# Optimization experiments

Measured on AMD Instinct MI355X. Metric: run time of the kernel, lower is better.

## Reference

```python
import jax, jax.numpy as jnp
import numpy as np

B, N, D = 8, 4096, 3

def setup_inputs() -> dict:
    key = jax.random.key(0)
    kx, ky = jax.random.split(key)
    x = jax.random.normal(kx, (B, N, D), dtype=jnp.float32)
    y = jax.random.normal(ky, (B, N, D), dtype=jnp.float32)
    return {"x": x, "y": y}

def _nn_diff(A, B_):
    # brute-force NN: squared distances [N, M] via ||a||^2 + ||b||^2 - 2 a.b
    a2 = jnp.sum(A * A, axis=-1)[:, None]
    b2 = jnp.sum(B_ * B_, axis=-1)[None, :]
    d2 = a2 + b2 - 2.0 * (A @ B_.T)
    idx = jnp.argmin(d2, axis=1)            # closest point in B_ for each point in A
    return A - B_[idx]                      # [N, D] signed residuals

def _sigma_pair(S1, S2):
    d12 = _nn_diff(S1, S2)                  # S1 -> S2 residuals
    d21 = _nn_diff(S2, S1)                  # S2 -> S1 residuals
    # torch.std over the whole [N, D] tensor with Bessel's correction (ddof=1)
    std1 = jnp.std(d12, ddof=1)
    std2 = jnp.std(d21, ddof=1)
    return jnp.maximum(std1, std2)

def reference(x, y):
    per_batch = jax.vmap(_sigma_pair)(x, y)  # [B]
    return per_batch.mean()
```

## Files before the change

kernel.cpp:

```cpp
#include <hip/hip_runtime.h>
#include <math.h>

#define NPTS 4096
#define BLK 256
#define NUNITS 16
#define QGRP 128
#define QGRPS 32
#define GRID1 (NUNITS * QGRPS)
#define PHT 2048
#define CNT 12288.0f

typedef _Float16 half8 __attribute__((ext_vector_type(8)));
typedef float f32x16 __attribute__((ext_vector_type(16)));

__device__ __forceinline__ unsigned umin2(unsigned a, unsigned b) { return a < b ? a : b; }
__device__ __forceinline__ float fmin3(float a, float b, float c) {
  return fminf(fminf(a, b), c);
}

__device__ __forceinline__ float tilemin16(const f32x16 d) {
  const float a0 = fmin3(d[0],  d[1],  d[2]);
  const float a1 = fmin3(d[3],  d[4],  d[5]);
  const float a2 = fmin3(d[6],  d[7],  d[8]);
  const float a3 = fmin3(d[9],  d[10], d[11]);
  const float a4 = fmin3(d[12], d[13], d[14]);
  return fminf(fmin3(a0, a1, a2), fmin3(a3, a4, d[15]));
}

__global__ __launch_bounds__(BLK, 2) void fullscan_kernel(
    const float* __restrict__ x, const float* __restrict__ y,
    float2* __restrict__ partials) {
  __shared__ half8 Ap[2 * PHT];
  __shared__ half8 Bq[2 * QGRP];
  __shared__ float wS[4], wSS[4];

  const int bid  = blockIdx.x;
  const int unit = bid >> 5, qg = bid & 31;
  const int b = unit >> 1, dir = unit & 1;
  const float* __restrict__ Q = (dir ? y : x) + (size_t)b * NPTS * 3;
  const float* __restrict__ T = (dir ? x : y) + (size_t)b * NPTS * 3;

  const int tid = threadIdx.x;
  const _Float16 one  = (_Float16)1.0f;
  const _Float16 zero = (_Float16)0.0f;
  const _Float16 n2   = (_Float16)(-2.0f);

  if (tid < QGRP) {
    const int qq = qg * QGRP + tid;
    const float ax = Q[3 * qq], ay = Q[3 * qq + 1], az = Q[3 * qq + 2];
    const float a2 = fmaf(ax, ax, fmaf(ay, ay, az * az));
    const _Float16 ah0 = (_Float16)ax, ah1 = (_Float16)ay, ah2 = (_Float16)az;
    const _Float16 al0 = (_Float16)(ax - (float)ah0);
    const _Float16 al1 = (_Float16)(ay - (float)ah1);
    const _Float16 al2 = (_Float16)(az - (float)ah2);
    const _Float16 a2h = (_Float16)a2;
    const _Float16 a2l = (_Float16)(a2 - (float)a2h);
    half8 lo, hi;
    lo[0] = n2 * ah0; lo[1] = n2 * ah1; lo[2] = n2 * ah2; lo[3] = n2 * ah0;
    lo[4] = n2 * ah1; lo[5] = n2 * ah2; lo[6] = n2 * al0; lo[7] = n2 * al1;
    hi[0] = n2 * al2; hi[1] = one; hi[2] = one; hi[3] = a2h;
    hi[4] = a2l; hi[5] = zero; hi[6] = zero; hi[7] = zero;
    Bq[tid]        = lo;
    Bq[QGRP + tid] = hi;
  }

  const int lane = tid & 63, w = tid >> 6, ln = lane & 31, hi5 = lane >> 5;
  unsigned kacc0 = 0xFFFFFFFFu, kacc1 = 0xFFFFFFFFu;
  f32x16 Z;
  #pragma unroll
  for (int r = 0; r < 16; ++r) Z[r] = 0.0f;

  half8 bf;
  for (int c = 0; c < 2; ++c) {
    __syncthreads();
    #pragma unroll
    for (int k = 0; k < 8; ++k) {
      const int i  = tid + k * BLK;
      const int tg = c * PHT + i;
      const float bx = T[3 * tg], by = T[3 * tg + 1], bz = T[3 * tg + 2];
      const float b2 = fmaf(bx, bx, fmaf(by, by, bz * bz));
      const _Float16 bh0 = (_Float16)bx, bh1 = (_Float16)by, bh2 = (_Float16)bz;
      const _Float16 bl0 = (_Float16)(bx - (float)bh0);
      const _Float16 bl1 = (_Float16)(by - (float)bh1);
      const _Float16 bl2 = (_Float16)(bz - (float)bh2);
      const _Float16 s2h = (_Float16)b2;
      const _Float16 s2l = (_Float16)(b2 - (float)s2h);
      half8 lo, hi;
      lo[0] = bh0; lo[1] = bh1; lo[2] = bh2; lo[3] = bl0;
      lo[4] = bl1; lo[5] = bl2; lo[6] = bh0; lo[7] = bh1;
      hi[0] = bh2; hi[1] = s2h; hi[2] = s2l; hi[3] = one;
      hi[4] = one; hi[5] = zero; hi[6] = zero; hi[7] = zero;
      Ap[i]       = lo;
      Ap[PHT + i] = hi;
    }
    __syncthreads();
    if (c == 0) bf = Bq[hi5 * QGRP + w * 32 + ln];

    const unsigned cb = (unsigned)(c * (PHT / 32));
    #pragma unroll 4
    for (int t = 0; t < PHT / 32; ++t) {
      const half8 af = Ap[hi5 * PHT + t * 32 + ln];
      const f32x16 d = __builtin_amdgcn_mfma_f32_32x32x16_f16(af, bf, Z, 0, 0, 0);
      const unsigned key = (__float_as_uint(tilemin16(d)) & 0xFFFFF000u) | (cb + (unsigned)t);
      if (t & 1) kacc1 = umin2(kacc1, key);
      else       kacc0 = umin2(kacc0, key);
    }
  }
  unsigned kacc = umin2(kacc0, kacc1);
  kacc = umin2(kacc, (unsigned)__shfl_xor((int)kacc, 32));

  float s = 0.f, ss = 0.f;
  if (lane < 32) {
    const int q = qg * QGRP + w * 32 + ln;
    const int tbase = (int)(kacc & 4095u) * 32;
    const float qx = Q[3 * q], qy = Q[3 * q + 1], qz = Q[3 * q + 2];
    unsigned best = 0xFFFFFFFFu;
    #pragma unroll 8
    for (int i = 0; i < 32; ++i) {
      const int j = tbase + i;
      const float dx = qx - T[3 * j];
      const float dy = qy - T[3 * j + 1];
      const float dz = qz - T[3 * j + 2];
      const float d2 = fmaf(dx, dx, fmaf(dy, dy, dz * dz));
      best = umin2(best, (__float_as_uint(d2) & 0xFFFFFFE0u) | (unsigned)i);
    }
    const int j = tbase + (int)(best & 31u);
    const float rx = qx - T[3 * j];
    const float ry = qy - T[3 * j + 1];
    const float rz = qz - T[3 * j + 2];
    s  = rx + ry + rz;
    ss = fmaf(rx, rx, fmaf(ry, ry, rz * rz));
  }

  #pragma unroll
  for (int off = 32; off > 0; off >>= 1) {
    s  += __shfl_down(s, off);
    ss += __shfl_down(ss, off);
  }
  if ((tid & 63) == 0) { wS[w] = s; wSS[w] = ss; }
  __syncthreads();
  if (tid == 0) {
    partials[bid] = make_float2(wS[0] + wS[1] + wS[2] + wS[3],
                                wSS[0] + wSS[1] + wSS[2] + wSS[3]);
  }
}

__global__ __launch_bounds__(BLK) void finalize_kernel(
    const float2* __restrict__ partials, float* __restrict__ out) {
  __shared__ float2 sh[GRID1];
  __shared__ float sig[NUNITS];

  sh[threadIdx.x]       = partials[threadIdx.x];
  sh[threadIdx.x + BLK] = partials[threadIdx.x + BLK];
  __syncthreads();

  if (threadIdx.x < NUNITS) {
    float S = 0.f, SS = 0.f;
    #pragma unroll
    for (int i = 0; i < QGRPS; ++i) {
      S  += sh[threadIdx.x * QGRPS + i].x;
      SS += sh[threadIdx.x * QGRPS + i].y;
    }
    const float var = (SS - S * S / CNT) / (CNT - 1.0f);
    sig[threadIdx.x] = sqrtf(fmaxf(var, 0.0f));
  }
  __syncthreads();

  if (threadIdx.x == 0) {
    float acc = 0.f;
    #pragma unroll
    for (int b = 0; b < 8; ++b) acc += fmaxf(sig[2 * b], sig[2 * b + 1]);
    out[0] = acc * 0.125f;
  }
}

extern "C" void kernel_launch(void* const* d_in, const int* in_sizes, int n_in,
                              void* d_out, int out_size, void* d_ws, size_t ws_size,
                              hipStream_t stream) {
  const float* x = (const float*)d_in[0];
  const float* y = (const float*)d_in[1];
  float* out = (float*)d_out;
  float2* partials = (float2*)d_ws;

  hipLaunchKernelGGL(fullscan_kernel, dim3(GRID1), dim3(BLK), 0, stream,
                     x, y, partials);
  hipLaunchKernelGGL(finalize_kernel, dim3(1), dim3(BLK), 0, stream,
                     partials, out);
}
```

Before: 23.30 us.

## Precompute fp16 MFMA operands in a pack kernel and prefetch target phases into registers

Adds a pack kernel that converts every point set once into its hi/lo fp16 MFMA operand layout. Before, each of the 512 blocks redid this conversion for all 4096 target points. The scan kernel now loads the packed operands and splits the targets into four phases of 1024. The next phase is prefetched into registers while the current phase's MFMAs run, which halves LDS use. In exchange it adds a kernel launch, about 2 MB of workspace traffic, and extra barriers per phase.

```diff
diff --git a/kernel.cpp b/kernel.cpp
--- a/kernel.cpp
+++ b/kernel.cpp
@@ -7,8 +7,11 @@
 #define QGRP 128
 #define QGRPS 32
 #define GRID1 (NUNITS * QGRPS)
-#define PHT 2048
+#define PHT 1024
+#define NPH 4
 #define CNT 12288.0f
+#define PACK_HALF8 (8 * 2 * 2 * 4096)
+#define PACK_BYTES ((size_t)PACK_HALF8 * 16)
 
 typedef _Float16 half8 __attribute__((ext_vector_type(8)));
 typedef float f32x16 __attribute__((ext_vector_type(16)));
@@ -27,8 +30,47 @@
   return fminf(fmin3(a0, a1, a2), fmin3(a3, a4, d[15]));
 }
 
+__global__ __launch_bounds__(BLK) void pack_kernel(
+    const float* __restrict__ x, const float* __restrict__ y,
+    half8* __restrict__ Apk, half8* __restrict__ Bpk) {
+  const int gid = blockIdx.x * BLK + threadIdx.x;
+  const int b   = gid >> 13;
+  const int set = (gid >> 12) & 1;
+  const int i   = gid & 4095;
+  const float* __restrict__ P = (set ? y : x) + (size_t)b * NPTS * 3;
+
+  const float px = P[3 * i], py = P[3 * i + 1], pz = P[3 * i + 2];
+  const float p2 = fmaf(px, px, fmaf(py, py, pz * pz));
+  const _Float16 h0 = (_Float16)px, h1 = (_Float16)py, h2 = (_Float16)pz;
+  const _Float16 l0 = (_Float16)(px - (float)h0);
+  const _Float16 l1 = (_Float16)(py - (float)h1);
+  const _Float16 l2 = (_Float16)(pz - (float)h2);
+  const _Float16 s2h = (_Float16)p2;
+  const _Float16 s2l = (_Float16)(p2 - (float)s2h);
+  const _Float16 one  = (_Float16)1.0f;
+  const _Float16 zero = (_Float16)0.0f;
+  const _Float16 n2   = (_Float16)(-2.0f);
+
+  half8 alo, ahi, blo, bhi;
+  alo[0] = h0; alo[1] = h1; alo[2] = h2; alo[3] = l0;
+  alo[4] = l1; alo[5] = l2; alo[6] = h0; alo[7] = h1;
+  ahi[0] = h2; ahi[1] = s2h; ahi[2] = s2l; ahi[3] = one;
+  ahi[4] = one; ahi[5] = zero; ahi[6] = zero; ahi[7] = zero;
+  blo[0] = n2 * h0; blo[1] = n2 * h1; blo[2] = n2 * h2; blo[3] = n2 * h0;
+  blo[4] = n2 * h1; blo[5] = n2 * h2; blo[6] = n2 * l0; blo[7] = n2 * l1;
+  bhi[0] = n2 * l2; bhi[1] = one; bhi[2] = one; bhi[3] = s2h;
+  bhi[4] = s2l; bhi[5] = zero; bhi[6] = zero; bhi[7] = zero;
+
+  const size_t base = (size_t)((b * 2 + set) * 2) * 4096 + i;
+  Apk[base]        = alo;
+  Apk[base + 4096] = ahi;
+  Bpk[base]        = blo;
+  Bpk[base + 4096] = bhi;
+}
+
 __global__ __launch_bounds__(BLK, 2) void fullscan_kernel(
     const float* __restrict__ x, const float* __restrict__ y,
+    const half8* __restrict__ Apk, const half8* __restrict__ Bpk,
     float2* __restrict__ partials) {
   __shared__ half8 Ap[2 * PHT];
   __shared__ half8 Bq[2 * QGRP];
@@ -39,71 +81,61 @@
   const int b = unit >> 1, dir = unit & 1;
   const float* __restrict__ Q = (dir ? y : x) + (size_t)b * NPTS * 3;
   const float* __restrict__ T = (dir ? x : y) + (size_t)b * NPTS * 3;
+  const half8* __restrict__ Ab = Apk + (size_t)((b * 2 + (1 - dir)) * 2) * 4096;
+  const half8* __restrict__ Bb = Bpk + (size_t)((b * 2 + dir) * 2) * 4096;
 
   const int tid = threadIdx.x;
-  const _Float16 one  = (_Float16)1.0f;
-  const _Float16 zero = (_Float16)0.0f;
-  const _Float16 n2   = (_Float16)(-2.0f);
-
-  if (tid < QGRP) {
-    const int qq = qg * QGRP + tid;
-    const float ax = Q[3 * qq], ay = Q[3 * qq + 1], az = Q[3 * qq + 2];
-    const float a2 = fmaf(ax, ax, fmaf(ay, ay, az * az));
-    const _Float16 ah0 = (_Float16)ax, ah1 = (_Float16)ay, ah2 = (_Float16)az;
-    const _Float16 al0 = (_Float16)(ax - (float)ah0);
-    const _Float16 al1 = (_Float16)(ay - (float)ah1);
-    const _Float16 al2 = (_Float16)(az - (float)ah2);
-    const _Float16 a2h = (_Float16)a2;
-    const _Float16 a2l = (_Float16)(a2 - (float)a2h);
-    half8 lo, hi;
-    lo[0] = n2 * ah0; lo[1] = n2 * ah1; lo[2] = n2 * ah2; lo[3] = n2 * ah0;
-    lo[4] = n2 * ah1; lo[5] = n2 * ah2; lo[6] = n2 * al0; lo[7] = n2 * al1;
-    hi[0] = n2 * al2; hi[1] = one; hi[2] = one; hi[3] = a2h;
-    hi[4] = a2l; hi[5] = zero; hi[6] = zero; hi[7] = zero;
-    Bq[tid]        = lo;
-    Bq[QGRP + tid] = hi;
-  }
+
+  {
+    const int plane = tid >> 7, qi = tid & 127;
+    Bq[plane * QGRP + qi] = Bb[(size_t)plane * 4096 + qg * QGRP + qi];
+  }
+  #pragma unroll
+  for (int k = 0; k < 8; ++k) {
+    const int e = k * BLK + tid;
+    const int plane = e >> 10, ti = e & 1023;
+    Ap[plane * PHT + ti] = Ab[(size_t)plane * 4096 + ti];
+  }
+  __syncthreads();
 
   const int lane = tid & 63, w = tid >> 6, ln = lane & 31, hi5 = lane >> 5;
-  unsigned kacc0 = 0xFFFFFFFFu, kacc1 = 0xFFFFFFFFu;
+  const half8 bf = Bq[hi5 * QGRP + w * 32 + ln];
+
   f32x16 Z;
   #pragma unroll
   for (int r = 0; r < 16; ++r) Z[r] = 0.0f;
 
-  half8 bf;
-  for (int c = 0; c < 2; ++c) {
-    __syncthreads();
-    #pragma unroll
-    for (int k = 0; k < 8; ++k) {
-      const int i  = tid + k * BLK;
-      const int tg = c * PHT + i;
-      const float bx = T[3 * tg], by = T[3 * tg + 1], bz = T[3 * tg + 2];
-      const float b2 = fmaf(bx, bx, fmaf(by, by, bz * bz));
-      const _Float16 bh0 = (_Float16)bx, bh1 = (_Float16)by, bh2 = (_Float16)bz;
-      const _Float16 bl0 = (_Float16)(bx - (float)bh0);
-      const _Float16 bl1 = (_Float16)(by - (float)bh1);
-      const _Float16 bl2 = (_Float16)(bz - (float)bh2);
-      const _Float16 s2h = (_Float16)b2;
-      const _Float16 s2l = (_Float16)(b2 - (float)s2h);
-      half8 lo, hi;
-      lo[0] = bh0; lo[1] = bh1; lo[2] = bh2; lo[3] = bl0;
-      lo[4] = bl1; lo[5] = bl2; lo[6] = bh0; lo[7] = bh1;
-      hi[0] = bh2; hi[1] = s2h; hi[2] = s2l; hi[3] = one;
-      hi[4] = one; hi[5] = zero; hi[6] = zero; hi[7] = zero;
-      Ap[i]       = lo;
-      Ap[PHT + i] = hi;
-    }
-    __syncthreads();
-    if (c == 0) bf = Bq[hi5 * QGRP + w * 32 + ln];
-
+  unsigned kacc0 = 0xFFFFFFFFu, kacc1 = 0xFFFFFFFFu;
+  half8 nxt[8];
+
+  for (int c = 0; c < NPH; ++c) {
+    if (c < NPH - 1) {
+      #pragma unroll
+      for (int k = 0; k < 8; ++k) {
+        const int e = k * BLK + tid;
+        const int plane = e >> 10, ti = e & 1023;
+        nxt[k] = Ab[(size_t)plane * 4096 + (c + 1) * PHT + ti];
+      }
+    }
     const unsigned cb = (unsigned)(c * (PHT / 32));
     #pragma unroll 4
     for (int t = 0; t < PHT / 32; ++t) {
       const half8 af = Ap[hi5 * PHT + t * 32 + ln];
       const f32x16 d = __builtin_amdgcn_mfma_f32_32x32x16_f16(af, bf, Z, 0, 0, 0);
-      const unsigned key = (__float_as_uint(tilemin16(d)) & 0xFFFFF000u) | (cb + (unsigned)t);
+      const unsigned key =
+          (__float_as_uint(tilemin16(d)) & 0xFFFFF000u) | (cb + (unsigned)t);
       if (t & 1) kacc1 = umin2(kacc1, key);
       else       kacc0 = umin2(kacc0, key);
+    }
+    __syncthreads();
+    if (c < NPH - 1) {
+      #pragma unroll
+      for (int k = 0; k < 8; ++k) {
+        const int e = k * BLK + tid;
+        const int plane = e >> 10, ti = e & 1023;
+        Ap[plane * PHT + ti] = nxt[k];
+      }
+      __syncthreads();
     }
   }
   unsigned kacc = umin2(kacc0, kacc1);
@@ -180,10 +212,16 @@
   const float* x = (const float*)d_in[0];
   const float* y = (const float*)d_in[1];
   float* out = (float*)d_out;
-  float2* partials = (float2*)d_ws;
-
+
+  char* ws = (char*)d_ws;
+  half8* Apk = (half8*)ws;
+  half8* Bpk = (half8*)(ws + PACK_BYTES);
+  float2* partials = (float2*)(ws + 2 * PACK_BYTES);
+
+  hipLaunchKernelGGL(pack_kernel, dim3(65536 / BLK), dim3(BLK), 0, stream,
+                     x, y, Apk, Bpk);
   hipLaunchKernelGGL(fullscan_kernel, dim3(GRID1), dim3(BLK), 0, stream,
-                     x, y, partials);
+                     x, y, Apk, Bpk, partials);
   hipLaunchKernelGGL(finalize_kernel, dim3(1), dim3(BLK), 0, stream,
                      partials, out);
 }
```

New measurement: 29.48 us. 26.6% more time.

## Split target scan across two waves per query tile with 512-thread blocks

Applied to the files above, without the earlier changes.

Doubles the block to 512 threads so that two waves share each 32-query tile, each scanning half of the target points in every chunk. Their packed min keys are merged through shared memory before a single wave refines the result. This halves the serial MFMA loop per wave and raises the number of waves in flight, which is meant to hide latency. The cost is an extra barrier plus shared-memory exchange, and higher register pressure because launch bounds now ask for 4 blocks of 512 threads.

```diff
diff --git a/kernel.cpp b/kernel.cpp
--- a/kernel.cpp
+++ b/kernel.cpp
@@ -2,7 +2,7 @@
 #include <math.h>
 
 #define NPTS 4096
-#define BLK 256
+#define BLK2 512
 #define NUNITS 16
 #define QGRP 128
 #define QGRPS 32
@@ -27,12 +27,13 @@
   return fminf(fmin3(a0, a1, a2), fmin3(a3, a4, d[15]));
 }
 
-__global__ __launch_bounds__(BLK, 2) void fullscan_kernel(
+__global__ __launch_bounds__(BLK2, 4) void fullscan_kernel(
     const float* __restrict__ x, const float* __restrict__ y,
     float2* __restrict__ partials) {
   __shared__ half8 Ap[2 * PHT];
   __shared__ half8 Bq[2 * QGRP];
-  __shared__ float wS[4], wSS[4];
+  __shared__ unsigned km[4][32];
+  __shared__ float wS[8], wSS[8];
 
   const int bid  = blockIdx.x;
   const int unit = bid >> 5, qg = bid & 31;
@@ -45,8 +46,9 @@
   const _Float16 zero = (_Float16)0.0f;
   const _Float16 n2   = (_Float16)(-2.0f);
 
-  if (tid < QGRP) {
-    const int qq = qg * QGRP + tid;
+  if (tid < 2 * QGRP) {
+    const int plane = tid >> 7, qi = tid & 127;
+    const int qq = qg * QGRP + qi;
     const float ax = Q[3 * qq], ay = Q[3 * qq + 1], az = Q[3 * qq + 2];
     const float a2 = fmaf(ax, ax, fmaf(ay, ay, az * az));
     const _Float16 ah0 = (_Float16)ax, ah1 = (_Float16)ay, ah2 = (_Float16)az;
@@ -55,16 +57,19 @@
     const _Float16 al2 = (_Float16)(az - (float)ah2);
     const _Float16 a2h = (_Float16)a2;
     const _Float16 a2l = (_Float16)(a2 - (float)a2h);
-    half8 lo, hi;
-    lo[0] = n2 * ah0; lo[1] = n2 * ah1; lo[2] = n2 * ah2; lo[3] = n2 * ah0;
-    lo[4] = n2 * ah1; lo[5] = n2 * ah2; lo[6] = n2 * al0; lo[7] = n2 * al1;
-    hi[0] = n2 * al2; hi[1] = one; hi[2] = one; hi[3] = a2h;
-    hi[4] = a2l; hi[5] = zero; hi[6] = zero; hi[7] = zero;
-    Bq[tid]        = lo;
-    Bq[QGRP + tid] = hi;
+    half8 v;
+    if (plane == 0) {
+      v[0] = n2 * ah0; v[1] = n2 * ah1; v[2] = n2 * ah2; v[3] = n2 * ah0;
+      v[4] = n2 * ah1; v[5] = n2 * ah2; v[6] = n2 * al0; v[7] = n2 * al1;
+    } else {
+      v[0] = n2 * al2; v[1] = one; v[2] = one; v[3] = a2h;
+      v[4] = a2l; v[5] = zero; v[6] = zero; v[7] = zero;
+    }
+    Bq[plane * QGRP + qi] = v;
   }
 
   const int lane = tid & 63, w = tid >> 6, ln = lane & 31, hi5 = lane >> 5;
+  const int qt = w >> 1, th = w & 1;
   unsigned kacc0 = 0xFFFFFFFFu, kacc1 = 0xFFFFFFFFu;
   f32x16 Z;
   #pragma unroll
@@ -74,8 +79,8 @@
   for (int c = 0; c < 2; ++c) {
     __syncthreads();
     #pragma unroll
-    for (int k = 0; k < 8; ++k) {
-      const int i  = tid + k * BLK;
+    for (int k = 0; k < 4; ++k) {
+      const int i  = tid + k * BLK2;
       const int tg = c * PHT + i;
       const float bx = T[3 * tg], by = T[3 * tg + 1], bz = T[3 * tg + 2];
       const float b2 = fmaf(bx, bx, fmaf(by, by, bz * bz));
@@ -94,14 +99,16 @@
       Ap[PHT + i] = hi;
     }
     __syncthreads();
-    if (c == 0) bf = Bq[hi5 * QGRP + w * 32 + ln];
-
-    const unsigned cb = (unsigned)(c * (PHT / 32));
+    if (c == 0) bf = Bq[hi5 * QGRP + qt * 32 + ln];
+
+    const unsigned cb = (unsigned)(c * 64 + th * 32);
+    const int abase = hi5 * PHT + th * 1024;
     #pragma unroll 4
-    for (int t = 0; t < PHT / 32; ++t) {
-      const half8 af = Ap[hi5 * PHT + t * 32 + ln];
+    for (int t = 0; t < 32; ++t) {
+      const half8 af = Ap[abase + t * 32 + ln];
       const f32x16 d = __builtin_amdgcn_mfma_f32_32x32x16_f16(af, bf, Z, 0, 0, 0);
-      const unsigned key = (__float_as_uint(tilemin16(d)) & 0xFFFFF000u) | (cb + (unsigned)t);
+      const unsigned key =
+          (__float_as_uint(tilemin16(d)) & 0xFFFFF000u) | (cb + (unsigned)t);
       if (t & 1) kacc1 = umin2(kacc1, key);
       else       kacc0 = umin2(kacc0, key);
     }
@@ -109,9 +116,13 @@
   unsigned kacc = umin2(kacc0, kacc1);
   kacc = umin2(kacc, (unsigned)__shfl_xor((int)kacc, 32));
 
+  if (th == 1 && lane < 32) km[qt][ln] = kacc;
+  __syncthreads();
+
   float s = 0.f, ss = 0.f;
-  if (lane < 32) {
-    const int q = qg * QGRP + w * 32 + ln;
+  if (th == 0 && lane < 32) {
+    kacc = umin2(kacc, km[qt][ln]);
+    const int q = qg * QGRP + qt * 32 + ln;
     const int tbase = (int)(kacc & 4095u) * 32;
     const float qx = Q[3 * q], qy = Q[3 * q + 1], qz = Q[3 * q + 2];
     unsigned best = 0xFFFFFFFFu;
@@ -140,18 +151,20 @@
   if ((tid & 63) == 0) { wS[w] = s; wSS[w] = ss; }
   __syncthreads();
   if (tid == 0) {
-    partials[bid] = make_float2(wS[0] + wS[1] + wS[2] + wS[3],
-                                wSS[0] + wSS[1] + wSS[2] + wSS[3]);
-  }
-}
-
-__global__ __launch_bounds__(BLK) void finalize_kernel(
+    float S = 0.f, SS = 0.f;
+    #pragma unroll
+    for (int i = 0; i < 8; ++i) { S += wS[i]; SS += wSS[i]; }
+    partials[bid] = make_float2(S, SS);
+  }
+}
+
+__global__ __launch_bounds__(256) void finalize_kernel(
     const float2* __restrict__ partials, float* __restrict__ out) {
   __shared__ float2 sh[GRID1];
   __shared__ float sig[NUNITS];
 
   sh[threadIdx.x]       = partials[threadIdx.x];
-  sh[threadIdx.x + BLK] = partials[threadIdx.x + BLK];
+  sh[threadIdx.x + 256] = partials[threadIdx.x + 256];
   __syncthreads();
 
   if (threadIdx.x < NUNITS) {
@@ -182,8 +195,8 @@
   float* out = (float*)d_out;
   float2* partials = (float2*)d_ws;
 
-  hipLaunchKernelGGL(fullscan_kernel, dim3(GRID1), dim3(BLK), 0, stream,
+  hipLaunchKernelGGL(fullscan_kernel, dim3(GRID1), dim3(BLK2), 0, stream,
                      x, y, partials);
-  hipLaunchKernelGGL(finalize_kernel, dim3(1), dim3(BLK), 0, stream,
+  hipLaunchKernelGGL(finalize_kernel, dim3(1), dim3(256), 0, stream,
                      partials, out);
 }
```

Measured after the change: 24.14 us. +3.6%, slower.
